# Optimization experiments

Measured on AMD Instinct MI355X. Metric: run time of the kernel, lower is better.

Reference implementation:

```python
import jax, jax.numpy as jnp
import numpy as np

DIM = 512
HEADS = 8
DIM_HEAD = 32
INNER = HEADS * DIM_HEAD  # 256
B, N = 2, 2048
EPS = 1e-5


def setup_inputs() -> dict:
    key = jax.random.key(0)
    ks = jax.random.split(key, 6)
    x = jax.random.normal(ks[0], (B, N, DIM), dtype=jnp.float32)
    rel_pos_bias = jax.random.normal(ks[1], (HEADS, N, N), dtype=jnp.float32)
    ln_scale = jnp.ones((DIM,), dtype=jnp.float32)
    w_qkv = jax.random.normal(ks[2], (DIM, INNER * 3), dtype=jnp.float32) / np.sqrt(DIM)
    w_out = jax.random.normal(ks[3], (INNER, DIM), dtype=jnp.float32) / np.sqrt(INNER)
    b_out = jnp.zeros((DIM,), dtype=jnp.float32)
    return {"x": x, "rel_pos_bias": rel_pos_bias, "ln_scale": ln_scale,
            "w_qkv": w_qkv, "w_out": w_out, "b_out": b_out}


def reference(x, rel_pos_bias, ln_scale, w_qkv, w_out, b_out):
    scale = DIM_HEAD ** -0.5
    # LayerNorm (no bias), eps=1e-5
    mu = jnp.mean(x, axis=-1, keepdims=True)
    var = jnp.mean(jnp.square(x - mu), axis=-1, keepdims=True)
    xn = (x - mu) * jax.lax.rsqrt(var + EPS) * ln_scale
    # fused QKV projection, no bias
    qkv = xn @ w_qkv  # [b, n, 3*inner]
    q, k, v = jnp.split(qkv, 3, axis=-1)
    def to_heads(t):
        b, n, _ = t.shape
        return t.reshape(b, n, HEADS, DIM_HEAD).transpose(0, 2, 1, 3)  # b h n d
    q, k, v = map(to_heads, (q, k, v))
    q = q * scale
    sim = jnp.einsum('bhid,bhjd->bhij', q, k)
    sim = sim + rel_pos_bias  # (h,n,n) broadcasts over batch
    attn = jax.nn.softmax(sim, axis=-1)
    o = jnp.einsum('bhij,bhjd->bhid', attn, v)
    o = o.transpose(0, 2, 1, 3).reshape(x.shape[0], x.shape[1], INNER)  # b n (h d)
    return o @ w_out + b_out
```

## Files before the change

### kernel.cpp

```cpp
#include <hip/hip_runtime.h>
#include <hip/hip_bf16.h>
#include <cstdint>

#define NB 2
#define NSEQ 2048
#define NDIM 512
#define NHEAD 8
#define DHEAD 32
#define NINNER 256
#define NQKV 768
#define LNEPS 1e-5f
#define QSCALE 0.17677669529663687f

typedef short short8 __attribute__((ext_vector_type(8)));
typedef float f32x4 __attribute__((ext_vector_type(4)));
typedef unsigned int u32x4 __attribute__((ext_vector_type(4)));
typedef unsigned int u32x2 __attribute__((ext_vector_type(2)));
typedef unsigned short u16;
typedef unsigned int u32;

__device__ __forceinline__ f32x4 mfma16(short8 a, short8 b, f32x4 c) {
    return __builtin_amdgcn_mfma_f32_16x16x32_bf16(a, b, c, 0, 0, 0);
}

__device__ __forceinline__ u16 f2bf(float a) {
    union { float f; u32 u; } x; x.f = a;
    u32 r = x.u + 0x7fffu + ((x.u >> 16) & 1u);
    return (u16)(r >> 16);
}
__device__ __forceinline__ float bf2f(u16 h) {
    union { float f; u32 u; } x; x.u = ((u32)h) << 16; return x.f;
}
__device__ __forceinline__ void split2(float a, u16& hi, u16& lo) {
    hi = f2bf(a);
    lo = f2bf(a - bf2f(hi));
}
__device__ __forceinline__ u32 pk2(float a, float b) {
    return (u32)f2bf(a) | ((u32)f2bf(b) << 16);
}

__global__ __launch_bounds__(256) void ln_kernel(
    const float* __restrict__ x, const float* __restrict__ gamma,
    u32* __restrict__ xn_hi, u32* __restrict__ xn_lo)
{
    const int row = blockIdx.x;
    const int t = threadIdx.x;
    const float2 v = ((const float2*)(x + (size_t)row * NDIM))[t];
    float s1 = v.x + v.y;
    float s2 = v.x * v.x + v.y * v.y;
    #pragma unroll
    for (int off = 32; off >= 1; off >>= 1) {
        s1 += __shfl_down(s1, off);
        s2 += __shfl_down(s2, off);
    }
    __shared__ float a1[4], a2[4];
    if ((t & 63) == 0) { a1[t >> 6] = s1; a2[t >> 6] = s2; }
    __syncthreads();
    const float ts1 = a1[0] + a1[1] + a1[2] + a1[3];
    const float ts2 = a2[0] + a2[1] + a2[2] + a2[3];
    const float mu = ts1 * (1.0f / NDIM);
    const float var = ts2 * (1.0f / NDIM) - mu * mu;
    const float rs = rsqrtf(var + LNEPS);
    const float2 g = ((const float2*)gamma)[t];
    u16 h0, l0, h1, l1;
    split2((v.x - mu) * rs * g.x, h0, l0);
    split2((v.y - mu) * rs * g.y, h1, l1);
    xn_hi[(size_t)row * (NDIM / 2) + t] = (u32)h0 | ((u32)h1 << 16);
    xn_lo[(size_t)row * (NDIM / 2) + t] = (u32)l0 | ((u32)l1 << 16);
}

__global__ __launch_bounds__(256) void wtrans_kernel(
    const float* __restrict__ wq, u16* __restrict__ wqT_hi, u16* __restrict__ wqT_lo,
    const float* __restrict__ wo, u16* __restrict__ woT_hi, u16* __restrict__ woT_lo)
{
    __shared__ __align__(16) u16 th[64][72], tl[64][72];
    const int t = threadIdx.x;
    const float* w; u16 *wT_hi, *wT_lo; int K, N, k0, n0;
    if (blockIdx.x < 96) {
        w = wq; wT_hi = wqT_hi; wT_lo = wqT_lo; K = NDIM; N = NQKV;
        k0 = (blockIdx.x & 7) * 64; n0 = (blockIdx.x >> 3) * 64;
    } else {
        const int b = blockIdx.x - 96;
        w = wo; wT_hi = woT_hi; wT_lo = woT_lo; K = NINNER; N = NDIM;
        k0 = (b & 3) * 64; n0 = (b >> 2) * 64;
    }
    {
        const int k = t >> 2, c = (t & 3) * 16;
        const float* src = w + (size_t)(k0 + k) * N + n0 + c;
        #pragma unroll
        for (int jj = 0; jj < 4; jj++) {
            const f32x4 w4 = *(const f32x4*)(src + jj * 4);
            #pragma unroll
            for (int e = 0; e < 4; e++) {
                u16 hh, ll;
                split2(w4[e], hh, ll);
                th[k][c + jj * 4 + e] = hh;
                tl[k][c + jj * 4 + e] = ll;
            }
        }
    }
    __syncthreads();
    {
        const int n = t >> 2, kc = (t & 3) * 16;
        u16 hb[16], lb[16];
        #pragma unroll
        for (int j = 0; j < 16; j++) { hb[j] = th[kc + j][n]; lb[j] = tl[kc + j][n]; }
        u16* dh = wT_hi + (size_t)(n0 + n) * K + k0 + kc;
        u16* dl = wT_lo + (size_t)(n0 + n) * K + k0 + kc;
        *(short8*)dh = *(short8*)hb;
        *(short8*)(dh + 8) = *(short8*)(hb + 8);
        *(short8*)dl = *(short8*)lb;
        *(short8*)(dl + 8) = *(short8*)(lb + 8);
    }
}

__global__ __launch_bounds__(256) void vtrans_kernel(
    const u16* __restrict__ v, u16* __restrict__ vt)
{
    __shared__ __align__(16) u16 sh[64][40];
    const int t = threadIdx.x;
    const int n0 = blockIdx.x * 64;
    const int bh = blockIdx.y;
    {
        const int n = t >> 2, c = (t & 3) * 8;
        *(short8*)&sh[n][c] = *(const short8*)(v + ((size_t)bh * NSEQ + n0 + n) * DHEAD + c);
    }
    __syncthreads();
    {
        const int d = t >> 3, nc = (t & 7) * 8;
        u16 buf[8];
        #pragma unroll
        for (int j = 0; j < 8; j++) buf[j] = sh[nc + j][d];
        *(short8*)(vt + ((size_t)bh * DHEAD + d) * NSEQ + n0 + nc) = *(short8*)buf;
    }
}

__global__ __launch_bounds__(256, 4) void qkv_kernel(
    const u16* __restrict__ xn_hi, const u16* __restrict__ xn_lo,
    const u16* __restrict__ wT_hi, const u16* __restrict__ wT_lo,
    u16* __restrict__ q_hi, u16* __restrict__ q_lo,
    u16* __restrict__ k_hi, u16* __restrict__ k_lo,
    u16* __restrict__ v)
{
    __shared__ __align__(16) u16 Ah[64][40], Al[64][40], Bh[64][40], Bl[64][40];
    const int t = threadIdx.x;
    const int wave = t >> 6, lane = t & 63;
    const int lrow = lane & 15, lquad = lane >> 4;
    const int rowBase = blockIdx.x * 64;
    const int colBase = blockIdx.y * 64;
    const int wm = (wave & 1) * 32;
    const int wn = (wave >> 1) * 32;
    const int kf = lquad * 8;
    const f32x4 zero = {0.f, 0.f, 0.f, 0.f};
    f32x4 acc[2][2];
    acc[0][0] = zero; acc[0][1] = zero; acc[1][0] = zero; acc[1][1] = zero;

    const int sr = t >> 2, sc = (t & 3) * 8;

    for (int k0 = 0; k0 < NDIM; k0 += 32) {
        __syncthreads();
        *(short8*)&Ah[sr][sc] = *(const short8*)(xn_hi + (size_t)(rowBase + sr) * NDIM + k0 + sc);
        *(short8*)&Al[sr][sc] = *(const short8*)(xn_lo + (size_t)(rowBase + sr) * NDIM + k0 + sc);
        *(short8*)&Bh[sr][sc] = *(const short8*)(wT_hi + (size_t)(colBase + sr) * NDIM + k0 + sc);
        *(short8*)&Bl[sr][sc] = *(const short8*)(wT_lo + (size_t)(colBase + sr) * NDIM + k0 + sc);
        __syncthreads();
        const short8 a0h = *(const short8*)&Ah[wm + lrow][kf];
        const short8 a0l = *(const short8*)&Al[wm + lrow][kf];
        const short8 a1h = *(const short8*)&Ah[wm + 16 + lrow][kf];
        const short8 a1l = *(const short8*)&Al[wm + 16 + lrow][kf];
        const short8 b0h = *(const short8*)&Bh[wn + lrow][kf];
        const short8 b0l = *(const short8*)&Bl[wn + lrow][kf];
        const short8 b1h = *(const short8*)&Bh[wn + 16 + lrow][kf];
        const short8 b1l = *(const short8*)&Bl[wn + 16 + lrow][kf];
        acc[0][0] = mfma16(a0h, b0h, acc[0][0]); acc[0][0] = mfma16(a0h, b0l, acc[0][0]); acc[0][0] = mfma16(a0l, b0h, acc[0][0]);
        acc[0][1] = mfma16(a0h, b1h, acc[0][1]); acc[0][1] = mfma16(a0h, b1l, acc[0][1]); acc[0][1] = mfma16(a0l, b1h, acc[0][1]);
        acc[1][0] = mfma16(a1h, b0h, acc[1][0]); acc[1][0] = mfma16(a1h, b0l, acc[1][0]); acc[1][0] = mfma16(a1l, b0h, acc[1][0]);
        acc[1][1] = mfma16(a1h, b1h, acc[1][1]); acc[1][1] = mfma16(a1h, b1l, acc[1][1]); acc[1][1] = mfma16(a1l, b1h, acc[1][1]);
    }

    #pragma unroll
    for (int mi = 0; mi < 2; mi++) {
        #pragma unroll
        for (int ni = 0; ni < 2; ni++) {
            #pragma unroll
            for (int r = 0; r < 4; r++) {
                const int grow = rowBase + wm + mi * 16 + lquad * 4 + r;
                const int gcol = colBase + wn + ni * 16 + lrow;
                const float val = acc[mi][ni][r];
                const int bidx = grow >> 11;
                const int n = grow & (NSEQ - 1);
                const int sec = gcol >> 8;
                const int idx = gcol & 255;
                const int head = idx >> 5, d = idx & 31;
                const int bh = bidx * NHEAD + head;
                if (sec == 0) {
                    u16 hh, ll;
                    split2(val * QSCALE, hh, ll);
                    const size_t a = ((size_t)bh * NSEQ + n) * DHEAD + d;
                    q_hi[a] = hh; q_lo[a] = ll;
                } else if (sec == 1) {
                    u16 hh, ll;
                    split2(val, hh, ll);
                    const size_t a = ((size_t)bh * NSEQ + n) * DHEAD + d;
                    k_hi[a] = hh; k_lo[a] = ll;
                } else {
                    v[((size_t)bh * NSEQ + n) * DHEAD + d] = f2bf(val);
                }
            }
        }
    }
}

__global__ __launch_bounds__(512, 8) void attn_kernel(
    const u16* __restrict__ q_hi, const u16* __restrict__ q_lo,
    const u16* __restrict__ k_hi, const u16* __restrict__ k_lo,
    const u16* __restrict__ vt,
    const float* __restrict__ bias,
    u16* __restrict__ o_hi, u16* __restrict__ o_lo)
{
    __shared__ __align__(16) float cA[2][4][64][4];
    __shared__ __align__(16) float cB[2][4][64][4];
    __shared__ float cl[2][4][16];
    const int t = threadIdx.x;
    const int wave = t >> 6, lane = t & 63;
    const int lrow = lane & 15, lquad = lane >> 4;
    const int batch = wave >> 2, wslice = wave & 3;
    const int head = blockIdx.y;
    const int qb = blockIdx.x * 16;
    const size_t qkb = (size_t)(batch * NHEAD + head) * NSEQ * DHEAD;
    const size_t qoff = (size_t)(qb + lrow) * DHEAD + lquad * 8;
    const short8 qh = *(const short8*)(q_hi + qkb + qoff);
    const short8 ql = *(const short8*)(q_lo + qkb + qoff);
    const f32x4 zero = {0.f, 0.f, 0.f, 0.f};
    f32x4 accA = zero, accB = zero;
    float lp = 0.f;
    const int kperm = ((lrow >> 2) << 3) | (lrow & 3);
    const float* bptr = bias + (size_t)head * NSEQ * NSEQ + (size_t)(qb + lrow) * NSEQ;
    const int kt0 = wslice * 512;

    for (int i = 0; i < 16; i++) {
        const int kt = kt0 + i * 32;
        const size_t kof = (size_t)(kt + kperm) * DHEAD + lquad * 8;
        const short8 k0h = *(const short8*)(k_hi + qkb + kof);
        const short8 k0l = *(const short8*)(k_lo + qkb + kof);
        const short8 k1h = *(const short8*)(k_hi + qkb + kof + 4 * DHEAD);
        const short8 k1l = *(const short8*)(k_lo + qkb + kof + 4 * DHEAD);
        const short8 va0 = *(const short8*)(vt + qkb + (size_t)lrow * NSEQ + kt + lquad * 8);
        const short8 va1 = *(const short8*)(vt + qkb + (size_t)(16 + lrow) * NSEQ + kt + lquad * 8);
        const f32x4 bias0 = *(const f32x4*)(bptr + kt + lquad * 8);
        const f32x4 bias1 = *(const f32x4*)(bptr + kt + lquad * 8 + 4);

        f32x4 c0 = zero, c1 = zero;
        c0 = mfma16(k0h, qh, c0); c0 = mfma16(k0h, ql, c0); c0 = mfma16(k0l, qh, c0);
        c1 = mfma16(k1h, qh, c1); c1 = mfma16(k1h, ql, c1); c1 = mfma16(k1l, qh, c1);
        f32x4 p0, p1;
        #pragma unroll
        for (int r = 0; r < 4; r++) {
            p0[r] = __expf(c0[r] + bias0[r]);
            p1[r] = __expf(c1[r] + bias1[r]);
        }
        lp += (p0[0] + p0[1]) + (p0[2] + p0[3]) + (p1[0] + p1[1]) + (p1[2] + p1[3]);
        union { u32x4 u; short8 s; } cv;
        cv.u[0] = pk2(p0[0], p0[1]);
        cv.u[1] = pk2(p0[2], p0[3]);
        cv.u[2] = pk2(p1[0], p1[1]);
        cv.u[3] = pk2(p1[2], p1[3]);
        accA = mfma16(va0, cv.s, accA);
        accB = mfma16(va1, cv.s, accB);
    }

    lp += __shfl_xor(lp, 16);
    lp += __shfl_xor(lp, 32);

    *(f32x4*)&cA[batch][wslice][lane][0] = accA;
    *(f32x4*)&cB[batch][wslice][lane][0] = accB;
    if (lquad == 0) cl[batch][wslice][lrow] = lp;
    __syncthreads();
    if (wslice == 0) {
        f32x4 sA = *(const f32x4*)&cA[batch][0][lane][0];
        f32x4 sB = *(const f32x4*)&cB[batch][0][lane][0];
        #pragma unroll
        for (int w = 1; w < 4; w++) {
            sA += *(const f32x4*)&cA[batch][w][lane][0];
            sB += *(const f32x4*)&cB[batch][w][lane][0];
        }
        const float lt = cl[batch][0][lrow] + cl[batch][1][lrow]
                       + cl[batch][2][lrow] + cl[batch][3][lrow];
        const float inv = 1.0f / lt;
        const size_t base = ((size_t)batch * NSEQ + qb + lrow) * NINNER + head * DHEAD + lquad * 4;
        u16 h[8], l[8];
        #pragma unroll
        for (int r = 0; r < 4; r++) {
            split2(sA[r] * inv, h[r], l[r]);
            split2(sB[r] * inv, h[4 + r], l[4 + r]);
        }
        *(u32x2*)&o_hi[base] = *(u32x2*)&h[0];
        *(u32x2*)&o_hi[base + 16] = *(u32x2*)&h[4];
        *(u32x2*)&o_lo[base] = *(u32x2*)&l[0];
        *(u32x2*)&o_lo[base + 16] = *(u32x2*)&l[4];
    }
}

__global__ __launch_bounds__(256, 4) void out_kernel(
    const u16* __restrict__ o_hi, const u16* __restrict__ o_lo,
    const u16* __restrict__ wT_hi, const u16* __restrict__ wT_lo,
    const float* __restrict__ b_out,
    float* __restrict__ out)
{
    __shared__ __align__(16) u16 Ah[64][40], Al[64][40], Bh[64][40], Bl[64][40];
    const int t = threadIdx.x;
    const int wave = t >> 6, lane = t & 63;
    const int lrow = lane & 15, lquad = lane >> 4;
    const int rowBase = blockIdx.x * 64;
    const int colBase = blockIdx.y * 64;
    const int wm = (wave & 1) * 32;
    const int wn = (wave >> 1) * 32;
    const int kf = lquad * 8;
    const f32x4 zero = {0.f, 0.f, 0.f, 0.f};
    f32x4 acc[2][2];
    acc[0][0] = zero; acc[0][1] = zero; acc[1][0] = zero; acc[1][1] = zero;

    const int sr = t >> 2, sc = (t & 3) * 8;

    for (int k0 = 0; k0 < NINNER; k0 += 32) {
        __syncthreads();
        *(short8*)&Ah[sr][sc] = *(const short8*)(o_hi + (size_t)(rowBase + sr) * NINNER + k0 + sc);
        *(short8*)&Al[sr][sc] = *(const short8*)(o_lo + (size_t)(rowBase + sr) * NINNER + k0 + sc);
        *(short8*)&Bh[sr][sc] = *(const short8*)(wT_hi + (size_t)(colBase + sr) * NINNER + k0 + sc);
        *(short8*)&Bl[sr][sc] = *(const short8*)(wT_lo + (size_t)(colBase + sr) * NINNER + k0 + sc);
        __syncthreads();
        const short8 a0h = *(const short8*)&Ah[wm + lrow][kf];
        const short8 a0l = *(const short8*)&Al[wm + lrow][kf];
        const short8 a1h = *(const short8*)&Ah[wm + 16 + lrow][kf];
        const short8 a1l = *(const short8*)&Al[wm + 16 + lrow][kf];
        const short8 b0h = *(const short8*)&Bh[wn + lrow][kf];
        const short8 b0l = *(const short8*)&Bl[wn + lrow][kf];
        const short8 b1h = *(const short8*)&Bh[wn + 16 + lrow][kf];
        const short8 b1l = *(const short8*)&Bl[wn + 16 + lrow][kf];
        acc[0][0] = mfma16(a0h, b0h, acc[0][0]); acc[0][0] = mfma16(a0h, b0l, acc[0][0]); acc[0][0] = mfma16(a0l, b0h, acc[0][0]);
        acc[0][1] = mfma16(a0h, b1h, acc[0][1]); acc[0][1] = mfma16(a0h, b1l, acc[0][1]); acc[0][1] = mfma16(a0l, b1h, acc[0][1]);
        acc[1][0] = mfma16(a1h, b0h, acc[1][0]); acc[1][0] = mfma16(a1h, b0l, acc[1][0]); acc[1][0] = mfma16(a1l, b0h, acc[1][0]);
        acc[1][1] = mfma16(a1h, b1h, acc[1][1]); acc[1][1] = mfma16(a1h, b1l, acc[1][1]); acc[1][1] = mfma16(a1l, b1h, acc[1][1]);
    }

    #pragma unroll
    for (int mi = 0; mi < 2; mi++) {
        #pragma unroll
        for (int ni = 0; ni < 2; ni++) {
            #pragma unroll
            for (int r = 0; r < 4; r++) {
                const int grow = rowBase + wm + mi * 16 + lquad * 4 + r;
                const int gcol = colBase + wn + ni * 16 + lrow;
                out[(size_t)grow * NDIM + gcol] = acc[mi][ni][r] + b_out[gcol];
            }
        }
    }
}

extern "C" void kernel_launch(void* const* d_in, const int* in_sizes, int n_in,
                              void* d_out, int out_size, void* d_ws, size_t ws_size,
                              hipStream_t stream)
{
    (void)in_sizes; (void)n_in; (void)out_size; (void)ws_size;
    const float* x     = (const float*)d_in[0];
    const float* bias  = (const float*)d_in[1];
    const float* gamma = (const float*)d_in[2];
    const float* wqkv  = (const float*)d_in[3];
    const float* wout  = (const float*)d_in[4];
    const float* bout  = (const float*)d_in[5];
    float* out = (float*)d_out;

    char* ws = (char*)d_ws;
    size_t off = 0;
    auto carve = [&](size_t bytes) -> void* {
        void* p = (void*)(ws + off);
        off += (bytes + 255) & ~(size_t)255;
        return p;
    };
    const size_t rows = (size_t)NB * NSEQ;
    const size_t hn = (size_t)NB * NHEAD * NSEQ * DHEAD;
    u16* xn_hi = (u16*)carve(rows * NDIM * 2);
    u16* xn_lo = (u16*)carve(rows * NDIM * 2);
    u16* wqT_hi = (u16*)carve((size_t)NQKV * NDIM * 2);
    u16* wqT_lo = (u16*)carve((size_t)NQKV * NDIM * 2);
    u16* woT_hi = (u16*)carve((size_t)NDIM * NINNER * 2);
    u16* woT_lo = (u16*)carve((size_t)NDIM * NINNER * 2);
    u16* q_hi  = (u16*)carve(hn * 2);
    u16* q_lo  = (u16*)carve(hn * 2);
    u16* k_hi  = (u16*)carve(hn * 2);
    u16* k_lo  = (u16*)carve(hn * 2);
    u16* vbuf  = (u16*)carve(hn * 2);
    u16* vt    = (u16*)carve(hn * 2);
    u16* o_hi  = (u16*)carve(rows * NINNER * 2);
    u16* o_lo  = (u16*)carve(rows * NINNER * 2);

    ln_kernel<<<dim3((unsigned)rows), 256, 0, stream>>>(x, gamma, (u32*)xn_hi, (u32*)xn_lo);
    wtrans_kernel<<<dim3(128), 256, 0, stream>>>(wqkv, wqT_hi, wqT_lo, wout, woT_hi, woT_lo);
    qkv_kernel<<<dim3(64, 12), 256, 0, stream>>>(xn_hi, xn_lo, wqT_hi, wqT_lo,
                                                 q_hi, q_lo, k_hi, k_lo, vbuf);
    vtrans_kernel<<<dim3(NSEQ / 64, NB * NHEAD), 256, 0, stream>>>(vbuf, vt);
    attn_kernel<<<dim3(128, 8), 512, 0, stream>>>(q_hi, q_lo, k_hi, k_lo,
                                                  vt, bias, o_hi, o_lo);
    out_kernel<<<dim3(64, 8), 256, 0, stream>>>(o_hi, o_lo, woT_hi, woT_lo, bout, out);
}
```

Measured before the change: 308.5 us.

## Process two query tiles per wave to reuse K/V loads and prefetch bias

The attention kernel now assigns one (batch, head) pair per block and has each wave handle 32 queries (two 16-row tiles) over a quarter of the keys, so every K and V fragment loaded from global memory feeds twice as many MFMAs. The grid changes from 128x8 to 32x16 and the launch-bounds occupancy hint drops to 4. Bias tiles for the next iteration are loaded one step ahead to hide their latency. The cost is higher register pressure and fewer blocks, which may lower occupancy. Bias is still read once per (batch, head), so the bias traffic, likely the dominant cost, is unchanged.

```diff
diff --git a/kernel.cpp b/kernel.cpp
--- a/kernel.cpp
+++ b/kernel.cpp
@@ -211,32 +211,42 @@
     }
 }
 
-__global__ __launch_bounds__(512, 8) void attn_kernel(
+__global__ __launch_bounds__(512, 4) void attn_kernel(
     const u16* __restrict__ q_hi, const u16* __restrict__ q_lo,
     const u16* __restrict__ k_hi, const u16* __restrict__ k_lo,
     const u16* __restrict__ vt,
     const float* __restrict__ bias,
     u16* __restrict__ o_hi, u16* __restrict__ o_lo)
 {
-    __shared__ __align__(16) float cA[2][4][64][4];
-    __shared__ __align__(16) float cB[2][4][64][4];
-    __shared__ float cl[2][4][16];
+    __shared__ __align__(16) float cA[2][2][4][64][4];
+    __shared__ __align__(16) float cB[2][2][4][64][4];
+    __shared__ float cl[2][2][4][16];
     const int t = threadIdx.x;
     const int wave = t >> 6, lane = t & 63;
     const int lrow = lane & 15, lquad = lane >> 4;
-    const int batch = wave >> 2, wslice = wave & 3;
-    const int head = blockIdx.y;
-    const int qb = blockIdx.x * 16;
-    const size_t qkb = (size_t)(batch * NHEAD + head) * NSEQ * DHEAD;
-    const size_t qoff = (size_t)(qb + lrow) * DHEAD + lquad * 8;
-    const short8 qh = *(const short8*)(q_hi + qkb + qoff);
-    const short8 ql = *(const short8*)(q_lo + qkb + qoff);
+    const int qpair = wave & 1, kslice = wave >> 1;
+    const int bh = blockIdx.y;
+    const int batch = bh >> 3, head = bh & 7;
+    const int qb = blockIdx.x * 64 + qpair * 32;
+    const size_t qkb = (size_t)bh * NSEQ * DHEAD;
+    const size_t qoff0 = (size_t)(qb + lrow) * DHEAD + lquad * 8;
+    const size_t qoff1 = (size_t)(qb + 16 + lrow) * DHEAD + lquad * 8;
+    const short8 qh0 = *(const short8*)(q_hi + qkb + qoff0);
+    const short8 ql0 = *(const short8*)(q_lo + qkb + qoff0);
+    const short8 qh1 = *(const short8*)(q_hi + qkb + qoff1);
+    const short8 ql1 = *(const short8*)(q_lo + qkb + qoff1);
     const f32x4 zero = {0.f, 0.f, 0.f, 0.f};
-    f32x4 accA = zero, accB = zero;
-    float lp = 0.f;
+    f32x4 accA0 = zero, accB0 = zero, accA1 = zero, accB1 = zero;
+    float lp0 = 0.f, lp1 = 0.f;
     const int kperm = ((lrow >> 2) << 3) | (lrow & 3);
-    const float* bptr = bias + (size_t)head * NSEQ * NSEQ + (size_t)(qb + lrow) * NSEQ;
-    const int kt0 = wslice * 512;
+    const float* bptr0 = bias + (size_t)head * NSEQ * NSEQ + (size_t)(qb + lrow) * NSEQ;
+    const float* bptr1 = bptr0 + 16 * NSEQ;
+    const int kt0 = kslice * 512;
+
+    f32x4 b00 = *(const f32x4*)(bptr0 + kt0 + lquad * 8);
+    f32x4 b01 = *(const f32x4*)(bptr0 + kt0 + lquad * 8 + 4);
+    f32x4 b10 = *(const f32x4*)(bptr1 + kt0 + lquad * 8);
+    f32x4 b11 = *(const f32x4*)(bptr1 + kt0 + lquad * 8 + 4);
 
     for (int i = 0; i < 16; i++) {
         const int kt = kt0 + i * 32;
@@ -247,47 +257,79 @@
         const short8 k1l = *(const short8*)(k_lo + qkb + kof + 4 * DHEAD);
         const short8 va0 = *(const short8*)(vt + qkb + (size_t)lrow * NSEQ + kt + lquad * 8);
         const short8 va1 = *(const short8*)(vt + qkb + (size_t)(16 + lrow) * NSEQ + kt + lquad * 8);
-        const f32x4 bias0 = *(const f32x4*)(bptr + kt + lquad * 8);
-        const f32x4 bias1 = *(const f32x4*)(bptr + kt + lquad * 8 + 4);
-
-        f32x4 c0 = zero, c1 = zero;
-        c0 = mfma16(k0h, qh, c0); c0 = mfma16(k0h, ql, c0); c0 = mfma16(k0l, qh, c0);
-        c1 = mfma16(k1h, qh, c1); c1 = mfma16(k1h, ql, c1); c1 = mfma16(k1l, qh, c1);
-        f32x4 p0, p1;
-        #pragma unroll
-        for (int r = 0; r < 4; r++) {
-            p0[r] = __expf(c0[r] + bias0[r]);
-            p1[r] = __expf(c1[r] + bias1[r]);
-        }
-        lp += (p0[0] + p0[1]) + (p0[2] + p0[3]) + (p1[0] + p1[1]) + (p1[2] + p1[3]);
-        union { u32x4 u; short8 s; } cv;
-        cv.u[0] = pk2(p0[0], p0[1]);
-        cv.u[1] = pk2(p0[2], p0[3]);
-        cv.u[2] = pk2(p1[0], p1[1]);
-        cv.u[3] = pk2(p1[2], p1[3]);
-        accA = mfma16(va0, cv.s, accA);
-        accB = mfma16(va1, cv.s, accB);
-    }
-
-    lp += __shfl_xor(lp, 16);
-    lp += __shfl_xor(lp, 32);
-
-    *(f32x4*)&cA[batch][wslice][lane][0] = accA;
-    *(f32x4*)&cB[batch][wslice][lane][0] = accB;
-    if (lquad == 0) cl[batch][wslice][lrow] = lp;
+        const int ktn = kt0 + ((i + 1) & 15) * 32;
+        const f32x4 nb00 = *(const f32x4*)(bptr0 + ktn + lquad * 8);
+        const f32x4 nb01 = *(const f32x4*)(bptr0 + ktn + lquad * 8 + 4);
+        const f32x4 nb10 = *(const f32x4*)(bptr1 + ktn + lquad * 8);
+        const f32x4 nb11 = *(const f32x4*)(bptr1 + ktn + lquad * 8 + 4);
+
+        {
+            f32x4 c0 = zero, c1 = zero;
+            c0 = mfma16(k0h, qh0, c0); c0 = mfma16(k0h, ql0, c0); c0 = mfma16(k0l, qh0, c0);
+            c1 = mfma16(k1h, qh0, c1); c1 = mfma16(k1h, ql0, c1); c1 = mfma16(k1l, qh0, c1);
+            f32x4 p0, p1;
+            #pragma unroll
+            for (int r = 0; r < 4; r++) {
+                p0[r] = __expf(c0[r] + b00[r]);
+                p1[r] = __expf(c1[r] + b01[r]);
+            }
+            lp0 += (p0[0] + p0[1]) + (p0[2] + p0[3]) + (p1[0] + p1[1]) + (p1[2] + p1[3]);
+            union { u32x4 u; short8 s; } cv;
+            cv.u[0] = pk2(p0[0], p0[1]);
+            cv.u[1] = pk2(p0[2], p0[3]);
+            cv.u[2] = pk2(p1[0], p1[1]);
+            cv.u[3] = pk2(p1[2], p1[3]);
+            accA0 = mfma16(va0, cv.s, accA0);
+            accB0 = mfma16(va1, cv.s, accB0);
+        }
+        {
+            f32x4 c0 = zero, c1 = zero;
+            c0 = mfma16(k0h, qh1, c0); c0 = mfma16(k0h, ql1, c0); c0 = mfma16(k0l, qh1, c0);
+            c1 = mfma16(k1h, qh1, c1); c1 = mfma16(k1h, ql1, c1); c1 = mfma16(k1l, qh1, c1);
+            f32x4 p0, p1;
+            #pragma unroll
+            for (int r = 0; r < 4; r++) {
+                p0[r] = __expf(c0[r] + b10[r]);
+                p1[r] = __expf(c1[r] + b11[r]);
+            }
+            lp1 += (p0[0] + p0[1]) + (p0[2] + p0[3]) + (p1[0] + p1[1]) + (p1[2] + p1[3]);
+            union { u32x4 u; short8 s; } cv;
+            cv.u[0] = pk2(p0[0], p0[1]);
+            cv.u[1] = pk2(p0[2], p0[3]);
+            cv.u[2] = pk2(p1[0], p1[1]);
+            cv.u[3] = pk2(p1[2], p1[3]);
+            accA1 = mfma16(va0, cv.s, accA1);
+            accB1 = mfma16(va1, cv.s, accB1);
+        }
+        b00 = nb00; b01 = nb01; b10 = nb10; b11 = nb11;
+    }
+
+    lp0 += __shfl_xor(lp0, 16); lp0 += __shfl_xor(lp0, 32);
+    lp1 += __shfl_xor(lp1, 16); lp1 += __shfl_xor(lp1, 32);
+
+    *(f32x4*)&cA[qpair][0][kslice][lane][0] = accA0;
+    *(f32x4*)&cB[qpair][0][kslice][lane][0] = accB0;
+    *(f32x4*)&cA[qpair][1][kslice][lane][0] = accA1;
+    *(f32x4*)&cB[qpair][1][kslice][lane][0] = accB1;
+    if (lquad == 0) {
+        cl[qpair][0][kslice][lrow] = lp0;
+        cl[qpair][1][kslice][lrow] = lp1;
+    }
     __syncthreads();
-    if (wslice == 0) {
-        f32x4 sA = *(const f32x4*)&cA[batch][0][lane][0];
-        f32x4 sB = *(const f32x4*)&cB[batch][0][lane][0];
+    if (wave < 4) {
+        const int qp = wave >> 1, s = wave & 1;
+        f32x4 sA = *(const f32x4*)&cA[qp][s][0][lane][0];
+        f32x4 sB = *(const f32x4*)&cB[qp][s][0][lane][0];
         #pragma unroll
         for (int w = 1; w < 4; w++) {
-            sA += *(const f32x4*)&cA[batch][w][lane][0];
-            sB += *(const f32x4*)&cB[batch][w][lane][0];
-        }
-        const float lt = cl[batch][0][lrow] + cl[batch][1][lrow]
-                       + cl[batch][2][lrow] + cl[batch][3][lrow];
+            sA += *(const f32x4*)&cA[qp][s][w][lane][0];
+            sB += *(const f32x4*)&cB[qp][s][w][lane][0];
+        }
+        const float lt = cl[qp][s][0][lrow] + cl[qp][s][1][lrow]
+                       + cl[qp][s][2][lrow] + cl[qp][s][3][lrow];
         const float inv = 1.0f / lt;
-        const size_t base = ((size_t)batch * NSEQ + qb + lrow) * NINNER + head * DHEAD + lquad * 4;
+        const int q = blockIdx.x * 64 + qp * 32 + s * 16 + lrow;
+        const size_t base = ((size_t)batch * NSEQ + q) * NINNER + head * DHEAD + lquad * 4;
         u16 h[8], l[8];
         #pragma unroll
         for (int r = 0; r < 4; r++) {
@@ -399,7 +441,7 @@
     qkv_kernel<<<dim3(64, 12), 256, 0, stream>>>(xn_hi, xn_lo, wqT_hi, wqT_lo,
                                                  q_hi, q_lo, k_hi, k_lo, vbuf);
     vtrans_kernel<<<dim3(NSEQ / 64, NB * NHEAD), 256, 0, stream>>>(vbuf, vt);
-    attn_kernel<<<dim3(128, 8), 512, 0, stream>>>(q_hi, q_lo, k_hi, k_lo,
+    attn_kernel<<<dim3(32, 16), 512, 0, stream>>>(q_hi, q_lo, k_hi, k_lo,
                                                   vt, bias, o_hi, o_lo);
     out_kernel<<<dim3(64, 8), 256, 0, stream>>>(o_hi, o_lo, woT_hi, woT_lo, bout, out);
 }
```

Measured after the change: 276.9 us. 1.11x faster.

## Restructure attention blocks per batch-head with 4 query tiles per wave and prefetch

Applied to the files above, without the earlier changes.

Each attention block now covers one batch-head and 128 queries, with each wave handling four 16-row query fragments so K and V^T loads are reused across them. K is stored only as a single bf16 (the k_lo term is dropped), cutting one MFMA per score tile and a buffer. The next iteration's K and bias tiles are software-prefetched, and bias loads use nontemporal hints. In exchange, register pressure goes up (launch bounds drop to 2 blocks), the bias is no longer shared across batches within a block, and dropping k_lo costs some accuracy.

```diff
diff --git a/kernel.cpp b/kernel.cpp
--- a/kernel.cpp
+++ b/kernel.cpp
@@ -139,7 +139,7 @@
     const u16* __restrict__ xn_hi, const u16* __restrict__ xn_lo,
     const u16* __restrict__ wT_hi, const u16* __restrict__ wT_lo,
     u16* __restrict__ q_hi, u16* __restrict__ q_lo,
-    u16* __restrict__ k_hi, u16* __restrict__ k_lo,
+    u16* __restrict__ k_hi,
     u16* __restrict__ v)
 {
     __shared__ __align__(16) u16 Ah[64][40], Al[64][40], Bh[64][40], Bl[64][40];
@@ -199,10 +199,7 @@
                     const size_t a = ((size_t)bh * NSEQ + n) * DHEAD + d;
                     q_hi[a] = hh; q_lo[a] = ll;
                 } else if (sec == 1) {
-                    u16 hh, ll;
-                    split2(val, hh, ll);
-                    const size_t a = ((size_t)bh * NSEQ + n) * DHEAD + d;
-                    k_hi[a] = hh; k_lo[a] = ll;
+                    k_hi[((size_t)bh * NSEQ + n) * DHEAD + d] = f2bf(val);
                 } else {
                     v[((size_t)bh * NSEQ + n) * DHEAD + d] = f2bf(val);
                 }
@@ -211,83 +208,120 @@
     }
 }
 
-__global__ __launch_bounds__(512, 8) void attn_kernel(
+__global__ __launch_bounds__(512, 2) void attn_kernel(
     const u16* __restrict__ q_hi, const u16* __restrict__ q_lo,
-    const u16* __restrict__ k_hi, const u16* __restrict__ k_lo,
+    const u16* __restrict__ k_hi,
     const u16* __restrict__ vt,
     const float* __restrict__ bias,
     u16* __restrict__ o_hi, u16* __restrict__ o_lo)
 {
-    __shared__ __align__(16) float cA[2][4][64][4];
-    __shared__ __align__(16) float cB[2][4][64][4];
-    __shared__ float cl[2][4][16];
+    __shared__ __align__(16) float cA[2][4][4][64][4];
+    __shared__ __align__(16) float cB[2][4][4][64][4];
+    __shared__ float cl[2][4][4][16];
     const int t = threadIdx.x;
     const int wave = t >> 6, lane = t & 63;
     const int lrow = lane & 15, lquad = lane >> 4;
-    const int batch = wave >> 2, wslice = wave & 3;
-    const int head = blockIdx.y;
-    const int qb = blockIdx.x * 16;
-    const size_t qkb = (size_t)(batch * NHEAD + head) * NSEQ * DHEAD;
-    const size_t qoff = (size_t)(qb + lrow) * DHEAD + lquad * 8;
-    const short8 qh = *(const short8*)(q_hi + qkb + qoff);
-    const short8 ql = *(const short8*)(q_lo + qkb + qoff);
+    const int qt = wave >> 2, ks = wave & 3;
+    const int bh = blockIdx.y;
+    const int batch = bh >> 3, head = bh & 7;
+    const int qbase = blockIdx.x * 128 + qt * 64;
+    const size_t qkb = (size_t)bh * NSEQ * DHEAD;
+
+    short8 qh[4], ql[4];
+    #pragma unroll
+    for (int f = 0; f < 4; f++) {
+        const size_t qoff = (size_t)(qbase + f * 16 + lrow) * DHEAD + lquad * 8;
+        qh[f] = *(const short8*)(q_hi + qkb + qoff);
+        ql[f] = *(const short8*)(q_lo + qkb + qoff);
+    }
     const f32x4 zero = {0.f, 0.f, 0.f, 0.f};
-    f32x4 accA = zero, accB = zero;
-    float lp = 0.f;
+    f32x4 accA[4], accB[4];
+    #pragma unroll
+    for (int f = 0; f < 4; f++) { accA[f] = zero; accB[f] = zero; }
+    float lp[4] = {0.f, 0.f, 0.f, 0.f};
     const int kperm = ((lrow >> 2) << 3) | (lrow & 3);
-    const float* bptr = bias + (size_t)head * NSEQ * NSEQ + (size_t)(qb + lrow) * NSEQ;
-    const int kt0 = wslice * 512;
+    const float* bp[4];
+    #pragma unroll
+    for (int f = 0; f < 4; f++)
+        bp[f] = bias + (size_t)head * NSEQ * NSEQ + (size_t)(qbase + f * 16 + lrow) * NSEQ;
+    const int kt0 = ks * 512;
+
+    short8 kc0 = *(const short8*)(k_hi + qkb + (size_t)(kt0 + kperm) * DHEAD + lquad * 8);
+    short8 kc1 = *(const short8*)(k_hi + qkb + (size_t)(kt0 + kperm + 4) * DHEAD + lquad * 8);
+    f32x4 bc0[4], bc1[4];
+    #pragma unroll
+    for (int f = 0; f < 4; f++) {
+        bc0[f] = __builtin_nontemporal_load((const f32x4*)(bp[f] + kt0 + lquad * 8));
+        bc1[f] = __builtin_nontemporal_load((const f32x4*)(bp[f] + kt0 + lquad * 8 + 4));
+    }
 
     for (int i = 0; i < 16; i++) {
         const int kt = kt0 + i * 32;
-        const size_t kof = (size_t)(kt + kperm) * DHEAD + lquad * 8;
-        const short8 k0h = *(const short8*)(k_hi + qkb + kof);
-        const short8 k0l = *(const short8*)(k_lo + qkb + kof);
-        const short8 k1h = *(const short8*)(k_hi + qkb + kof + 4 * DHEAD);
-        const short8 k1l = *(const short8*)(k_lo + qkb + kof + 4 * DHEAD);
+        const int ktn = kt0 + ((i + 1) & 15) * 32;
+        const short8 kn0 = *(const short8*)(k_hi + qkb + (size_t)(ktn + kperm) * DHEAD + lquad * 8);
+        const short8 kn1 = *(const short8*)(k_hi + qkb + (size_t)(ktn + kperm + 4) * DHEAD + lquad * 8);
         const short8 va0 = *(const short8*)(vt + qkb + (size_t)lrow * NSEQ + kt + lquad * 8);
         const short8 va1 = *(const short8*)(vt + qkb + (size_t)(16 + lrow) * NSEQ + kt + lquad * 8);
-        const f32x4 bias0 = *(const f32x4*)(bptr + kt + lquad * 8);
-        const f32x4 bias1 = *(const f32x4*)(bptr + kt + lquad * 8 + 4);
-
-        f32x4 c0 = zero, c1 = zero;
-        c0 = mfma16(k0h, qh, c0); c0 = mfma16(k0h, ql, c0); c0 = mfma16(k0l, qh, c0);
-        c1 = mfma16(k1h, qh, c1); c1 = mfma16(k1h, ql, c1); c1 = mfma16(k1l, qh, c1);
-        f32x4 p0, p1;
-        #pragma unroll
-        for (int r = 0; r < 4; r++) {
-            p0[r] = __expf(c0[r] + bias0[r]);
-            p1[r] = __expf(c1[r] + bias1[r]);
-        }
-        lp += (p0[0] + p0[1]) + (p0[2] + p0[3]) + (p1[0] + p1[1]) + (p1[2] + p1[3]);
-        union { u32x4 u; short8 s; } cv;
-        cv.u[0] = pk2(p0[0], p0[1]);
-        cv.u[1] = pk2(p0[2], p0[3]);
-        cv.u[2] = pk2(p1[0], p1[1]);
-        cv.u[3] = pk2(p1[2], p1[3]);
-        accA = mfma16(va0, cv.s, accA);
-        accB = mfma16(va1, cv.s, accB);
-    }
-
-    lp += __shfl_xor(lp, 16);
-    lp += __shfl_xor(lp, 32);
-
-    *(f32x4*)&cA[batch][wslice][lane][0] = accA;
-    *(f32x4*)&cB[batch][wslice][lane][0] = accB;
-    if (lquad == 0) cl[batch][wslice][lrow] = lp;
+        f32x4 bn0[4], bn1[4];
+        #pragma unroll
+        for (int f = 0; f < 4; f++) {
+            bn0[f] = __builtin_nontemporal_load((const f32x4*)(bp[f] + ktn + lquad * 8));
+            bn1[f] = __builtin_nontemporal_load((const f32x4*)(bp[f] + ktn + lquad * 8 + 4));
+        }
+        #pragma unroll
+        for (int f = 0; f < 4; f++) {
+            f32x4 c0 = zero, c1 = zero;
+            c0 = mfma16(kc0, qh[f], c0); c0 = mfma16(kc0, ql[f], c0);
+            c1 = mfma16(kc1, qh[f], c1); c1 = mfma16(kc1, ql[f], c1);
+            f32x4 p0, p1;
+            #pragma unroll
+            for (int r = 0; r < 4; r++) {
+                p0[r] = __expf(c0[r] + bc0[f][r]);
+                p1[r] = __expf(c1[r] + bc1[f][r]);
+            }
+            lp[f] += (p0[0] + p0[1]) + (p0[2] + p0[3]) + (p1[0] + p1[1]) + (p1[2] + p1[3]);
+            union { u32x4 u; short8 s; } cv;
+            cv.u[0] = pk2(p0[0], p0[1]);
+            cv.u[1] = pk2(p0[2], p0[3]);
+            cv.u[2] = pk2(p1[0], p1[1]);
+            cv.u[3] = pk2(p1[2], p1[3]);
+            accA[f] = mfma16(va0, cv.s, accA[f]);
+            accB[f] = mfma16(va1, cv.s, accB[f]);
+        }
+        kc0 = kn0; kc1 = kn1;
+        #pragma unroll
+        for (int f = 0; f < 4; f++) { bc0[f] = bn0[f]; bc1[f] = bn1[f]; }
+    }
+
+    #pragma unroll
+    for (int f = 0; f < 4; f++) {
+        lp[f] += __shfl_xor(lp[f], 16);
+        lp[f] += __shfl_xor(lp[f], 32);
+    }
+    #pragma unroll
+    for (int f = 0; f < 4; f++) {
+        *(f32x4*)&cA[qt][ks][f][lane][0] = accA[f];
+        *(f32x4*)&cB[qt][ks][f][lane][0] = accB[f];
+    }
+    if (lquad == 0) {
+        #pragma unroll
+        for (int f = 0; f < 4; f++) cl[qt][ks][f][lrow] = lp[f];
+    }
     __syncthreads();
-    if (wslice == 0) {
-        f32x4 sA = *(const f32x4*)&cA[batch][0][lane][0];
-        f32x4 sB = *(const f32x4*)&cB[batch][0][lane][0];
+    {
+        const int oqt = wave >> 2, of = wave & 3;
+        f32x4 sA = *(const f32x4*)&cA[oqt][0][of][lane][0];
+        f32x4 sB = *(const f32x4*)&cB[oqt][0][of][lane][0];
         #pragma unroll
         for (int w = 1; w < 4; w++) {
-            sA += *(const f32x4*)&cA[batch][w][lane][0];
-            sB += *(const f32x4*)&cB[batch][w][lane][0];
-        }
-        const float lt = cl[batch][0][lrow] + cl[batch][1][lrow]
-                       + cl[batch][2][lrow] + cl[batch][3][lrow];
+            sA += *(const f32x4*)&cA[oqt][w][of][lane][0];
+            sB += *(const f32x4*)&cB[oqt][w][of][lane][0];
+        }
+        const float lt = cl[oqt][0][of][lrow] + cl[oqt][1][of][lrow]
+                       + cl[oqt][2][of][lrow] + cl[oqt][3][of][lrow];
         const float inv = 1.0f / lt;
-        const size_t base = ((size_t)batch * NSEQ + qb + lrow) * NINNER + head * DHEAD + lquad * 4;
+        const int q = blockIdx.x * 128 + oqt * 64 + of * 16 + lrow;
+        const size_t base = ((size_t)batch * NSEQ + q) * NINNER + head * DHEAD + lquad * 4;
         u16 h[8], l[8];
         #pragma unroll
         for (int r = 0; r < 4; r++) {
@@ -388,7 +422,6 @@
     u16* q_hi  = (u16*)carve(hn * 2);
     u16* q_lo  = (u16*)carve(hn * 2);
     u16* k_hi  = (u16*)carve(hn * 2);
-    u16* k_lo  = (u16*)carve(hn * 2);
     u16* vbuf  = (u16*)carve(hn * 2);
     u16* vt    = (u16*)carve(hn * 2);
     u16* o_hi  = (u16*)carve(rows * NINNER * 2);
@@ -397,9 +430,9 @@
     ln_kernel<<<dim3((unsigned)rows), 256, 0, stream>>>(x, gamma, (u32*)xn_hi, (u32*)xn_lo);
     wtrans_kernel<<<dim3(128), 256, 0, stream>>>(wqkv, wqT_hi, wqT_lo, wout, woT_hi, woT_lo);
     qkv_kernel<<<dim3(64, 12), 256, 0, stream>>>(xn_hi, xn_lo, wqT_hi, wqT_lo,
-                                                 q_hi, q_lo, k_hi, k_lo, vbuf);
+                                                 q_hi, q_lo, k_hi, vbuf);
     vtrans_kernel<<<dim3(NSEQ / 64, NB * NHEAD), 256, 0, stream>>>(vbuf, vt);
-    attn_kernel<<<dim3(128, 8), 512, 0, stream>>>(q_hi, q_lo, k_hi, k_lo,
+    attn_kernel<<<dim3(16, 16), 512, 0, stream>>>(q_hi, q_lo, k_hi,
                                                   vt, bias, o_hi, o_lo);
     out_kernel<<<dim3(64, 8), 256, 0, stream>>>(o_hi, o_lo, woT_hi, woT_lo, bout, out);
 }
```

After: 291.6 us. -5.5%, faster.
